# Kernel tuning notes

Measured on AMD Instinct MI355X. Metric: run time of the kernel, lower is better.

The kernel has to match this reference:

```python
import jax, jax.numpy as jnp
import numpy as np

STATE_DIM = 1024
INPUT_DIM = 256
OUTPUT_DIM = 256
KX = 10
LAM = 5.0
BSZ = 16
SEQ = 2048


def setup_inputs() -> dict:
    key = jax.random.key(0)
    ks = jax.random.split(key, 6)
    inputs = jax.random.normal(ks[0], (BSZ, SEQ, INPUT_DIM), dtype=jnp.float32)
    h0 = jax.random.normal(ks[1], (STATE_DIM,), dtype=jnp.float32)
    # exponential_decay_init: entries in (exp(-lam), 1)
    A = jnp.exp(-LAM * jax.random.uniform(ks[2], (STATE_DIM,), dtype=jnp.float32))
    B = jax.random.normal(ks[3], (INPUT_DIM, STATE_DIM), dtype=jnp.float32) / INPUT_DIM
    C = jax.random.normal(ks[4], (STATE_DIM, OUTPUT_DIM), dtype=jnp.float32) / STATE_DIM
    M = jax.random.normal(ks[5], (OUTPUT_DIM, INPUT_DIM, KX), dtype=jnp.float32) / OUTPUT_DIM
    return {"inputs": inputs, "h0": h0, "A": A, "B": B, "C": C, "M": M}


def _lds_forward(inputs, h0, A, B, C, M):
    bsz, L, _ = inputs.shape
    S = A.shape[0]
    kx = M.shape[-1]
    # input projection: u_t @ B  -> [B, L, S]
    uB = jnp.einsum('bld,ds->bls', inputs, B)
    # diagonal linear recurrence h_t = A * h_{t-1} + uB_t, h_{-1} = h0,
    # via parallel associative scan on affine maps (a, b): h -> a*h + b
    a = jnp.broadcast_to(A, (1, L, S))

    def combine(x, y):
        a1, b1 = x
        a2, b2 = y
        return (a1 * a2, a2 * b1 + b2)

    Pa, Pb = jax.lax.associative_scan(combine, (a, uB), axis=1)
    all_h = Pa * h0 + Pb                              # [B, L, S]
    lds_out = jnp.einsum('bls,so->blo', all_h, C)      # [B, L, O]
    # shift forward by kx: new[:, :-kx] = lds_out[:, kx:], tail zeros
    new_lds = jnp.pad(lds_out[:, kx:, :], ((0, 0), (0, kx), (0, 0)))
    # AR term: ar[b,t,o] = sum_{i<kx} M[o,:,i] . x[b, t-i, :] (zero-padded past)
    ar = jnp.zeros_like(new_lds)
    for i in range(kx):
        x_i = jnp.pad(inputs, ((0, 0), (i, 0), (0, 0)))[:, :L, :]
        ar = ar + jnp.einsum('oj,blj->blo', M[:, :, i], x_i)
    return ar + new_lds


def reference(inputs, h0, A, B, C, M):
    return _lds_forward(inputs, h0, A, B, C, M)
```

## Files before the change

kernel.cpp:

```cpp
#include <hip/hip_runtime.h>

#define BSZn 16
#define SEQn 2048
#define DIN 256
#define DST 1024
#define DOUTn 256
#define KXn 10
#define TCH 64
#define NCH 32

typedef __attribute__((ext_vector_type(4))) float f32x4;
typedef __attribute__((ext_vector_type(8))) short bf16x8;

__device__ __forceinline__ unsigned short f2bf(float f){
  unsigned u = __float_as_uint(f);
  u += 0x7FFF + ((u>>16)&1);
  return (unsigned short)(u>>16);
}
__device__ __forceinline__ float bf2f(unsigned short s){
  return __uint_as_float(((unsigned)s)<<16);
}

#define XIDX(r,c) ((((r)<<8) + (c)) ^ (((r)&7)<<3))


__global__ void k_prep(const float* __restrict__ B, const float* __restrict__ C,
                       const float* __restrict__ M, unsigned short* __restrict__ Bt2,
                       unsigned short* __restrict__ Ct2, unsigned short* __restrict__ Mt2){
  int stride = gridDim.x*blockDim.x;
  int i0 = blockIdx.x*blockDim.x + threadIdx.x;
  for(int idx=i0; idx<DIN*DST; idx+=stride){
    int d = idx>>10, s = idx&1023;
    Bt2[((d>>5)<<15) + (s<<5) + (d&31)] = f2bf(B[idx]);
  }
  for(int idx=i0; idx<DST*DOUTn; idx+=stride){
    int s = idx>>8, o = idx&255;
    Ct2[((s>>5)<<13) + (o<<5) + (s&31)] = f2bf(C[idx]);
  }
  for(int idx=i0; idx<DOUTn*DIN*KXn; idx+=stride){
    int q = idx/KXn, ii = idx - q*KXn;
    int o = q>>8, j = q&255;
    int k = (ii<<8) + j;
    Mt2[((k>>5)<<13) + (o<<5) + (k&31)] = f2bf(M[idx]);
  }
}

__global__ __launch_bounds__(256) void k_ub(const float* __restrict__ x,
    const unsigned short* __restrict__ Bt2, const float* __restrict__ A,
    unsigned short* __restrict__ uB, float* __restrict__ P){
  __shared__ __align__(16) unsigned short xt[64*256];
  int wg = blockIdx.x;
  int q = wg & 3, c = (wg>>2)&31, b = wg>>7;
  int t0 = c*TCH, s0 = q<<8;
  const float* xb = x + (size_t)b*SEQn*DIN;
  int tid = threadIdx.x;
  for(int e = tid; e < 64*64; e += 256){
    int r = e>>6, c4 = (e&63)<<2;
    float4 v = *(const float4*)(xb + (t0+r)*DIN + c4);
    ushort4 w; w.x=f2bf(v.x); w.y=f2bf(v.y); w.z=f2bf(v.z); w.w=f2bf(v.w);
    *(ushort4*)&xt[XIDX(r,c4)] = w;
  }
  __syncthreads();
  int wv = tid>>6, ln = tid&63, lm = ln&15, lk = (ln>>4)<<3, rr = (ln>>4)<<2;
  f32x4 zf = {0.f,0.f,0.f,0.f};
  f32x4 acc[4][4];
  #pragma unroll
  for(int tt=0;tt<4;tt++)
    #pragma unroll
    for(int nt=0;nt<4;nt++) acc[tt][nt] = zf;
  #pragma unroll
  for(int kb=0;kb<8;kb++){
    bf16x8 af[4];
    #pragma unroll
    for(int tt=0;tt<4;tt++)
      af[tt] = *(const bf16x8*)&xt[XIDX((tt<<4)+lm, (kb<<5)+lk)];
    #pragma unroll
    for(int nt=0;nt<4;nt++){
      int sg = s0 + (wv<<6) + (nt<<4) + lm;
      bf16x8 bfr = *(const bf16x8*)&Bt2[(kb<<15) + (sg<<5) + lk];
      #pragma unroll
      for(int tt=0;tt<4;tt++)
        acc[tt][nt] = __builtin_amdgcn_mfma_f32_16x16x32_bf16(af[tt], bfr, acc[tt][nt], 0,0,0);
    }
  }
  __syncthreads();
  #pragma unroll
  for(int tt=0;tt<4;tt++)
    #pragma unroll
    for(int nt=0;nt<4;nt++)
      #pragma unroll
      for(int r4=0;r4<4;r4++)
        xt[XIDX((tt<<4)+rr+r4, (wv<<6)+(nt<<4)+lm)] = f2bf(acc[tt][nt][r4]);
  __syncthreads();
  unsigned short* hb = uB + ((size_t)b*129)*32*512;
  #pragma unroll
  for(int it=0; it<8; it++){
    int j = it*256 + tid;
    int r = j>>5, c0 = (j&31)<<3;
    bf16x8 v = *(const bf16x8*)&xt[XIDX(r,c0)];
    int s = s0 + c0;
    size_t addr = (((size_t)(c*4 + (r>>4)))*32 + (s>>5))*512 + ((r&15)<<5) + (s&31);
    *(bf16x8*)&hb[addr] = v;
  }
  if(c == 31){
    unsigned* zp = (unsigned*)(uB + (((size_t)b*129 + 128)*32 + (q<<3))*512);
    for(int e = tid; e < 2048; e += 256) zp[e] = 0u;
  }
  {
    int s = s0 + tid;
    float Av = A[s];
    float p = 0.f;
    #pragma unroll
    for(int t=0;t<64;t++)
      p = fmaf(Av, p, bf2f(xt[XIDX(t, tid)]));
    P[(((b<<5)+c)<<10) + s] = p;
  }
}

__global__ __launch_bounds__(256) void k_h(unsigned short* __restrict__ uB,
    const float* __restrict__ A, const float* __restrict__ h0,
    const float* __restrict__ P){
  int wg = blockIdx.x;
  int half = wg & 1, c = (wg>>1) & 31, b = wg >> 6;
  int tid = threadIdx.x;
  int s = (half<<9) + (tid<<1);
  float2 Av = *(const float2*)(A + s);
  float a0 = Av.x, a1 = Av.y;
  #pragma unroll
  for(int sq=0;sq<6;sq++){ a0 *= a0; a1 *= a1; }
  float2 hv = *(const float2*)(h0 + s);
  float h0v = hv.x, h1v = hv.y;
  const float2* Pb = (const float2*)(P + (((size_t)(b<<5))<<10) + s);
  for(int j=0;j<c;j++){
    float2 pv = Pb[(size_t)j<<9];
    h0v = fmaf(a0, h0v, pv.x);
    h1v = fmaf(a1, h1v, pv.y);
  }
  unsigned short* hb = uB + (((size_t)b*129 + c*4)*32 + (s>>5))*512 + (s&31);
  #pragma unroll 4
  for(int t=0;t<64;t++){
    unsigned* p = (unsigned*)(hb + ((t>>4)*32*512) + ((t&15)<<5));
    unsigned v = *p;
    h0v = fmaf(Av.x, h0v, bf2f((unsigned short)(v & 0xffff)));
    h1v = fmaf(Av.y, h1v, bf2f((unsigned short)(v >> 16)));
    *p = (unsigned)f2bf(h0v) | (((unsigned)f2bf(h1v))<<16);
  }
}

__global__ __launch_bounds__(256,2) void k_arc(const float* __restrict__ x,
    const unsigned short* __restrict__ Mt2, const unsigned short* __restrict__ Ct2,
    const unsigned short* __restrict__ h2, float* __restrict__ out){
  __shared__ __align__(16) unsigned short xt[73*256];
  int wg = blockIdx.x;
  int b = wg>>5, c = wg&31;
  int t0 = c*TCH;
  const float* xb = x + (size_t)b*SEQn*DIN;
  int tid = threadIdx.x;
  for(int e = tid; e < 73*64; e += 256){
    int r = e>>6, c4 = (e&63)<<2;
    int t = t0 - 9 + r;
    float4 v = {0.f,0.f,0.f,0.f};
    if(t >= 0) v = *(const float4*)(xb + t*DIN + c4);
    ushort4 w; w.x=f2bf(v.x); w.y=f2bf(v.y); w.z=f2bf(v.z); w.w=f2bf(v.w);
    *(ushort4*)&xt[XIDX(r, c4)] = w;
  }
  __syncthreads();
  int wv = tid>>6, ln = tid&63, lm = ln&15, lk = (ln>>4)<<3, rr = (ln>>4)<<2;
  f32x4 zf = {0.f,0.f,0.f,0.f};
  f32x4 acc[4][4];
  #pragma unroll
  for(int tt=0;tt<4;tt++)
    #pragma unroll
    for(int nt=0;nt<4;nt++) acc[tt][nt] = zf;
  #pragma unroll 2
  for(int i=0;i<KXn;i++){
    #pragma unroll
    for(int kb8=0;kb8<8;kb8++){
      int col = (kb8<<5) + lk;
      int kq = i*8 + kb8;
      bf16x8 af[4];
      #pragma unroll
      for(int tt=0;tt<4;tt++)
        af[tt] = *(const bf16x8*)&xt[XIDX((tt<<4)+lm + 9 - i, col)];
      #pragma unroll
      for(int nt=0;nt<4;nt++){
        int o = (wv<<6) + (nt<<4) + lm;
        bf16x8 bfr = *(const bf16x8*)&Mt2[(kq<<13) + (o<<5) + lk];
        #pragma unroll
        for(int tt=0;tt<4;tt++)
          acc[tt][nt] = __builtin_amdgcn_mfma_f32_16x16x32_bf16(af[tt], bfr, acc[tt][nt], 0,0,0);
      }
    }
  }
  const unsigned short* hb = h2 + (size_t)b*129*32*512;
  int Tg0 = c*4 + (lm>=6 ? 1 : 0);
  int rowin = (lm<6) ? (10+lm) : (lm-6);
  #pragma unroll
  for(int kb=0;kb<32;kb++){
    bf16x8 af[4];
    #pragma unroll
    for(int tt=0;tt<4;tt++)
      af[tt] = *(const bf16x8*)&hb[(((size_t)(Tg0+tt))*32 + kb)*512 + rowin*32 + lk];
    #pragma unroll
    for(int nt=0;nt<4;nt++){
      int o = (wv<<6) + (nt<<4) + lm;
      bf16x8 bfr = *(const bf16x8*)&Ct2[(kb<<13) + (o<<5) + lk];
      #pragma unroll
      for(int tt=0;tt<4;tt++)
        acc[tt][nt] = __builtin_amdgcn_mfma_f32_16x16x32_bf16(af[tt], bfr, acc[tt][nt], 0,0,0);
    }
  }
  #pragma unroll
  for(int tt=0;tt<4;tt++)
    #pragma unroll
    for(int nt=0;nt<4;nt++)
      #pragma unroll
      for(int r4=0;r4<4;r4++){
        int m = (tt<<4) + rr + r4;
        int o = (wv<<6) + (nt<<4) + lm;
        out[((size_t)b*SEQn + t0 + m)*DOUTn + o] = acc[tt][nt][r4];
      }
}

extern "C" void kernel_launch(void* const* d_in, const int* in_sizes, int n_in,
                              void* d_out, int out_size, void* d_ws, size_t ws_size,
                              hipStream_t stream){
  const float* x  = (const float*)d_in[0];
  const float* h0 = (const float*)d_in[1];
  const float* A  = (const float*)d_in[2];
  const float* B  = (const float*)d_in[3];
  const float* C  = (const float*)d_in[4];
  const float* M  = (const float*)d_in[5];
  float* out = (float*)d_out;
  unsigned short* Bt2 = (unsigned short*)d_ws;
  unsigned short* Ct2 = Bt2 + DIN*DST;
  unsigned short* Mt2 = Ct2 + DST*DOUTn;
  float* P     = (float*)((char*)d_ws + ( 4u<<20));
  unsigned short* uB = (unsigned short*)((char*)d_ws + (8u<<20));
  k_prep <<<512, 256, 0, stream>>>(B, C, M, Bt2, Ct2, Mt2);
  k_ub   <<<BSZn*NCH*4, 256, 0, stream>>>(x, Bt2, A, uB, P);
  k_h    <<<BSZn*NCH*2, 256, 0, stream>>>(uB, A, h0, P);
  k_arc  <<<BSZn*NCH, 256, 0, stream>>>(x, Mt2, Ct2, uB, out);
}
```

Baseline: 255.8 us.

## Reuse x tile across state quarters in k_ub and double-buffer global loads in k_arc

k_ub now has each workgroup loop over all four 256-wide state quarters, so the x tile is loaded and converted to bf16 once instead of four times. Results are staged in a separate LDS buffer, which doubles shared memory per block and cuts the grid by 4x, lowering parallelism. In k_arc, the M and C/h operand loads from global memory are software-pipelined with explicit ping-pong register buffers so they overlap the MFMA work. This raises register pressure under the launch_bounds(256,2) limit.

```diff
diff --git a/kernel.cpp b/kernel.cpp
--- a/kernel.cpp
+++ b/kernel.cpp
@@ -49,9 +49,10 @@
     const unsigned short* __restrict__ Bt2, const float* __restrict__ A,
     unsigned short* __restrict__ uB, float* __restrict__ P){
   __shared__ __align__(16) unsigned short xt[64*256];
+  __shared__ __align__(16) unsigned short ub[64*256];
   int wg = blockIdx.x;
-  int q = wg & 3, c = (wg>>2)&31, b = wg>>7;
-  int t0 = c*TCH, s0 = q<<8;
+  int c = wg & 31, b = wg >> 5;
+  int t0 = c*TCH;
   const float* xb = x + (size_t)b*SEQn*DIN;
   int tid = threadIdx.x;
   for(int e = tid; e < 64*64; e += 256){
@@ -62,58 +63,61 @@
   }
   __syncthreads();
   int wv = tid>>6, ln = tid&63, lm = ln&15, lk = (ln>>4)<<3, rr = (ln>>4)<<2;
+  unsigned short* hb = uB + ((size_t)b*129)*32*512;
   f32x4 zf = {0.f,0.f,0.f,0.f};
-  f32x4 acc[4][4];
-  #pragma unroll
-  for(int tt=0;tt<4;tt++)
-    #pragma unroll
-    for(int nt=0;nt<4;nt++) acc[tt][nt] = zf;
-  #pragma unroll
-  for(int kb=0;kb<8;kb++){
-    bf16x8 af[4];
+  for(int q=0;q<4;q++){
+    int s0 = q<<8;
+    f32x4 acc[4][4];
     #pragma unroll
     for(int tt=0;tt<4;tt++)
-      af[tt] = *(const bf16x8*)&xt[XIDX((tt<<4)+lm, (kb<<5)+lk)];
-    #pragma unroll
-    for(int nt=0;nt<4;nt++){
-      int sg = s0 + (wv<<6) + (nt<<4) + lm;
-      bf16x8 bfr = *(const bf16x8*)&Bt2[(kb<<15) + (sg<<5) + lk];
+      #pragma unroll
+      for(int nt=0;nt<4;nt++) acc[tt][nt] = zf;
+    #pragma unroll
+    for(int kb=0;kb<8;kb++){
+      bf16x8 af[4];
       #pragma unroll
       for(int tt=0;tt<4;tt++)
-        acc[tt][nt] = __builtin_amdgcn_mfma_f32_16x16x32_bf16(af[tt], bfr, acc[tt][nt], 0,0,0);
+        af[tt] = *(const bf16x8*)&xt[XIDX((tt<<4)+lm, (kb<<5)+lk)];
+      #pragma unroll
+      for(int nt=0;nt<4;nt++){
+        int sg = s0 + (wv<<6) + (nt<<4) + lm;
+        bf16x8 bfr = *(const bf16x8*)&Bt2[(kb<<15) + (sg<<5) + lk];
+        #pragma unroll
+        for(int tt=0;tt<4;tt++)
+          acc[tt][nt] = __builtin_amdgcn_mfma_f32_16x16x32_bf16(af[tt], bfr, acc[tt][nt], 0,0,0);
+      }
     }
-  }
-  __syncthreads();
-  #pragma unroll
-  for(int tt=0;tt<4;tt++)
-    #pragma unroll
-    for(int nt=0;nt<4;nt++)
-      #pragma unroll
-      for(int r4=0;r4<4;r4++)
-        xt[XIDX((tt<<4)+rr+r4, (wv<<6)+(nt<<4)+lm)] = f2bf(acc[tt][nt][r4]);
-  __syncthreads();
-  unsigned short* hb = uB + ((size_t)b*129)*32*512;
-  #pragma unroll
-  for(int it=0; it<8; it++){
-    int j = it*256 + tid;
-    int r = j>>5, c0 = (j&31)<<3;
-    bf16x8 v = *(const bf16x8*)&xt[XIDX(r,c0)];
-    int s = s0 + c0;
-    size_t addr = (((size_t)(c*4 + (r>>4)))*32 + (s>>5))*512 + ((r&15)<<5) + (s&31);
-    *(bf16x8*)&hb[addr] = v;
+    __syncthreads();
+    #pragma unroll
+    for(int tt=0;tt<4;tt++)
+      #pragma unroll
+      for(int nt=0;nt<4;nt++)
+        #pragma unroll
+        for(int r4=0;r4<4;r4++)
+          ub[XIDX((tt<<4)+rr+r4, (wv<<6)+(nt<<4)+lm)] = f2bf(acc[tt][nt][r4]);
+    __syncthreads();
+    #pragma unroll
+    for(int it=0; it<8; it++){
+      int j = it*256 + tid;
+      int r = j>>5, c0 = (j&31)<<3;
+      bf16x8 v = *(const bf16x8*)&ub[XIDX(r,c0)];
+      int s = s0 + c0;
+      size_t addr = (((size_t)(c*4 + (r>>4)))*32 + (s>>5))*512 + ((r&15)<<5) + (s&31);
+      *(bf16x8*)&hb[addr] = v;
+    }
+    {
+      int s = s0 + tid;
+      float Av = A[s];
+      float p = 0.f;
+      #pragma unroll
+      for(int t=0;t<64;t++)
+        p = fmaf(Av, p, bf2f(ub[XIDX(t, tid)]));
+      P[(((b<<5)+c)<<10) + s] = p;
+    }
   }
   if(c == 31){
-    unsigned* zp = (unsigned*)(uB + (((size_t)b*129 + 128)*32 + (q<<3))*512);
-    for(int e = tid; e < 2048; e += 256) zp[e] = 0u;
-  }
-  {
-    int s = s0 + tid;
-    float Av = A[s];
-    float p = 0.f;
-    #pragma unroll
-    for(int t=0;t<64;t++)
-      p = fmaf(Av, p, bf2f(xt[XIDX(t, tid)]));
-    P[(((b<<5)+c)<<10) + s] = p;
+    unsigned* zp = (unsigned*)(uB + (((size_t)b*129 + 128)*32)*512);
+    for(int e = tid; e < 8192; e += 256) zp[e] = 0u;
   }
 }
 
@@ -172,44 +176,53 @@
   for(int tt=0;tt<4;tt++)
     #pragma unroll
     for(int nt=0;nt<4;nt++) acc[tt][nt] = zf;
-  #pragma unroll 2
-  for(int i=0;i<KXn;i++){
-    #pragma unroll
-    for(int kb8=0;kb8<8;kb8++){
-      int col = (kb8<<5) + lk;
-      int kq = i*8 + kb8;
-      bf16x8 af[4];
-      #pragma unroll
-      for(int tt=0;tt<4;tt++)
-        af[tt] = *(const bf16x8*)&xt[XIDX((tt<<4)+lm + 9 - i, col)];
-      #pragma unroll
-      for(int nt=0;nt<4;nt++){
-        int o = (wv<<6) + (nt<<4) + lm;
-        bf16x8 bfr = *(const bf16x8*)&Mt2[(kq<<13) + (o<<5) + lk];
-        #pragma unroll
-        for(int tt=0;tt<4;tt++)
-          acc[tt][nt] = __builtin_amdgcn_mfma_f32_16x16x32_bf16(af[tt], bfr, acc[tt][nt], 0,0,0);
-      }
-    }
-  }
+
+  const unsigned short* mb = Mt2 + ((((wv<<6)+lm)<<5) + lk);
+  bf16x8 pA[8], pB[8];
+#define LOADG(buf, IT0) { _Pragma("unroll") \
+    for(int j=0;j<8;j++){ int itt=(IT0)+(j>>2); \
+      buf[j] = *(const bf16x8*)&mb[((size_t)itt<<13) + ((j&3)<<9)]; } }
+#define COMPG(buf, IT0) { _Pragma("unroll") \
+    for(int jj=0;jj<2;jj++){ int itc=(IT0)+jj; int ii=itc>>3, k8=itc&7; \
+      int col=(k8<<5)+lk; bf16x8 af[4]; \
+      _Pragma("unroll") for(int tt=0;tt<4;tt++) \
+        af[tt] = *(const bf16x8*)&xt[XIDX((tt<<4)+lm+9-ii, col)]; \
+      _Pragma("unroll") for(int nt=0;nt<4;nt++){ \
+        _Pragma("unroll") for(int tt=0;tt<4;tt++) \
+          acc[tt][nt] = __builtin_amdgcn_mfma_f32_16x16x32_bf16(af[tt], buf[jj*4+nt], acc[tt][nt],0,0,0); } } }
+  LOADG(pA, 0)
+  for(int g=0; g<80; g+=4){
+    LOADG(pB, g+2)
+    COMPG(pA, g)
+    if(g+4 < 80) LOADG(pA, g+4)
+    COMPG(pB, g+2)
+  }
+
   const unsigned short* hb = h2 + (size_t)b*129*32*512;
   int Tg0 = c*4 + (lm>=6 ? 1 : 0);
   int rowin = (lm<6) ? (10+lm) : (lm-6);
-  #pragma unroll
-  for(int kb=0;kb<32;kb++){
-    bf16x8 af[4];
-    #pragma unroll
-    for(int tt=0;tt<4;tt++)
-      af[tt] = *(const bf16x8*)&hb[(((size_t)(Tg0+tt))*32 + kb)*512 + rowin*32 + lk];
-    #pragma unroll
-    for(int nt=0;nt<4;nt++){
-      int o = (wv<<6) + (nt<<4) + lm;
-      bf16x8 bfr = *(const bf16x8*)&Ct2[(kb<<13) + (o<<5) + lk];
-      #pragma unroll
-      for(int tt=0;tt<4;tt++)
-        acc[tt][nt] = __builtin_amdgcn_mfma_f32_16x16x32_bf16(af[tt], bfr, acc[tt][nt], 0,0,0);
-    }
-  }
+  const unsigned short* hp[4];
+  #pragma unroll
+  for(int tt=0;tt<4;tt++)
+    hp[tt] = hb + (((size_t)(Tg0+tt)*32)<<9) + rowin*32 + lk;
+  const unsigned short* cb = Ct2 + ((((wv<<6)+lm)<<5) + lk);
+  bf16x8 qa[4], qb4[4], qaf[4], qbf[4];
+#define CLOADG(bufA, bufB, KB) { _Pragma("unroll") \
+    for(int tt=0;tt<4;tt++) bufA[tt] = *(const bf16x8*)&hp[tt][((size_t)(KB))<<9]; \
+    _Pragma("unroll") \
+    for(int nt=0;nt<4;nt++) bufB[nt] = *(const bf16x8*)&cb[(((size_t)(KB))<<13) + (nt<<9)]; }
+#define CCOMP(bufA, bufB) { _Pragma("unroll") \
+    for(int nt=0;nt<4;nt++) \
+      _Pragma("unroll") for(int tt=0;tt<4;tt++) \
+        acc[tt][nt] = __builtin_amdgcn_mfma_f32_16x16x32_bf16(bufA[tt], bufB[nt], acc[tt][nt],0,0,0); }
+  CLOADG(qaf, qbf, 0)
+  for(int kb=0; kb<32; kb+=2){
+    CLOADG(qa, qb4, kb+1)
+    CCOMP(qaf, qbf)
+    if(kb+2 < 32) CLOADG(qaf, qbf, kb+2)
+    CCOMP(qa, qb4)
+  }
+
   #pragma unroll
   for(int tt=0;tt<4;tt++)
     #pragma unroll
@@ -238,7 +251,7 @@
   float* P     = (float*)((char*)d_ws + ( 4u<<20));
   unsigned short* uB = (unsigned short*)((char*)d_ws + (8u<<20));
   k_prep <<<512, 256, 0, stream>>>(B, C, M, Bt2, Ct2, Mt2);
-  k_ub   <<<BSZn*NCH*4, 256, 0, stream>>>(x, Bt2, A, uB, P);
+  k_ub   <<<BSZn*NCH, 256, 0, stream>>>(x, Bt2, A, uB, P);
   k_h    <<<BSZn*NCH*2, 256, 0, stream>>>(uB, A, h0, P);
   k_arc  <<<BSZn*NCH, 256, 0, stream>>>(x, Mt2, Ct2, uB, out);
 }
```

New measurement: 252.2 us. Within noise of the previous version (-1.4%).

## Stage weight tiles into LDS via async global_load_lds with double buffering

Applied to the files above, without the earlier changes.

Reorganizes the B, M and C weights into swizzled 8K-element tiles, with M and C concatenated into one stream. k_ub and k_arc now copy each tile into LDS with global_load_lds while the previous tile feeds MFMA, instead of reading weight fragments directly from global memory. k_ub is also restructured so one block handles all four state quarters and reuses its converted x tile, cutting the grid by four. This trades direct global loads for a barrier on every k-step, extra LDS use, and lower parallelism in k_ub.

```diff
diff --git a/kernel.cpp b/kernel.cpp
--- a/kernel.cpp
+++ b/kernel.cpp
@@ -20,38 +20,49 @@
 __device__ __forceinline__ float bf2f(unsigned short s){
   return __uint_as_float(((unsigned)s)<<16);
 }
+__device__ __forceinline__ void gl_lds16(const unsigned short* g, unsigned short* l){
+  __builtin_amdgcn_global_load_lds(
+      (const __attribute__((address_space(1))) void*)g,
+      (__attribute__((address_space(3))) void*)l, 16, 0, 0);
+}
 
 #define XIDX(r,c) ((((r)<<8) + (c)) ^ (((r)&7)<<3))
 
 
+
 __global__ void k_prep(const float* __restrict__ B, const float* __restrict__ C,
-                       const float* __restrict__ M, unsigned short* __restrict__ Bt2,
-                       unsigned short* __restrict__ Ct2, unsigned short* __restrict__ Mt2){
+                       const float* __restrict__ M, unsigned short* __restrict__ Ut,
+                       unsigned short* __restrict__ Wt){
   int stride = gridDim.x*blockDim.x;
   int i0 = blockIdx.x*blockDim.x + threadIdx.x;
   for(int idx=i0; idx<DIN*DST; idx+=stride){
     int d = idx>>10, s = idx&1023;
-    Bt2[((d>>5)<<15) + (s<<5) + (d&31)] = f2bf(B[idx]);
-  }
-  for(int idx=i0; idx<DST*DOUTn; idx+=stride){
-    int s = idx>>8, o = idx&255;
-    Ct2[((s>>5)<<13) + (o<<5) + (s&31)] = f2bf(C[idx]);
+    int sl = s&255, kl = d&31;
+    Ut[(size_t)(((s>>8)<<3)+(d>>5))*8192 + (sl<<5) + ((((kl>>3))^(sl&3))<<3) + (kl&7)]
+      = f2bf(B[idx]);
   }
   for(int idx=i0; idx<DOUTn*DIN*KXn; idx+=stride){
     int q = idx/KXn, ii = idx - q*KXn;
     int o = q>>8, j = q&255;
-    int k = (ii<<8) + j;
-    Mt2[((k>>5)<<13) + (o<<5) + (k&31)] = f2bf(M[idx]);
+    int kq = ii*8 + (j>>5), kl = j&31;
+    Wt[(size_t)kq*8192 + (o<<5) + (((kl>>3)^(o&3))<<3) + (kl&7)] = f2bf(M[idx]);
+  }
+  for(int idx=i0; idx<DST*DOUTn; idx+=stride){
+    int s = idx>>8, o = idx&255;
+    int kq = 80 + (s>>5), kl = s&31;
+    Wt[(size_t)kq*8192 + (o<<5) + (((kl>>3)^(o&3))<<3) + (kl&7)] = f2bf(C[idx]);
   }
 }
 
 __global__ __launch_bounds__(256) void k_ub(const float* __restrict__ x,
-    const unsigned short* __restrict__ Bt2, const float* __restrict__ A,
+    const unsigned short* __restrict__ Ut, const float* __restrict__ A,
     unsigned short* __restrict__ uB, float* __restrict__ P){
   __shared__ __align__(16) unsigned short xt[64*256];
+  __shared__ __align__(16) unsigned short sh[2][8192];
+  unsigned short* ubp = &sh[0][0];
   int wg = blockIdx.x;
-  int q = wg & 3, c = (wg>>2)&31, b = wg>>7;
-  int t0 = c*TCH, s0 = q<<8;
+  int c = wg & 31, b = wg >> 5;
+  int t0 = c*TCH;
   const float* xb = x + (size_t)b*SEQn*DIN;
   int tid = threadIdx.x;
   for(int e = tid; e < 64*64; e += 256){
@@ -60,60 +71,76 @@
     ushort4 w; w.x=f2bf(v.x); w.y=f2bf(v.y); w.z=f2bf(v.z); w.w=f2bf(v.w);
     *(ushort4*)&xt[XIDX(r,c4)] = w;
   }
-  __syncthreads();
   int wv = tid>>6, ln = tid&63, lm = ln&15, lk = (ln>>4)<<3, rr = (ln>>4)<<2;
+  int swz = ((ln>>4) ^ (lm&3)) << 3;
+  unsigned short* hb = uB + ((size_t)b*129)*32*512;
   f32x4 zf = {0.f,0.f,0.f,0.f};
-  f32x4 acc[4][4];
-  #pragma unroll
-  for(int tt=0;tt<4;tt++)
-    #pragma unroll
-    for(int nt=0;nt<4;nt++) acc[tt][nt] = zf;
-  #pragma unroll
-  for(int kb=0;kb<8;kb++){
-    bf16x8 af[4];
+  for(int q=0;q<4;q++){
+    int s0 = q<<8;
+    __syncthreads();
+    {
+      const unsigned short* src = Ut + (size_t)(q<<3)*8192;
+      #pragma unroll
+      for(int i=0;i<4;i++){ int ci=(i<<2)+wv; gl_lds16(src+ci*512+ln*8, &sh[0][ci*512]); }
+    }
+    __syncthreads();
+    f32x4 acc[4][4];
     #pragma unroll
     for(int tt=0;tt<4;tt++)
-      af[tt] = *(const bf16x8*)&xt[XIDX((tt<<4)+lm, (kb<<5)+lk)];
-    #pragma unroll
-    for(int nt=0;nt<4;nt++){
-      int sg = s0 + (wv<<6) + (nt<<4) + lm;
-      bf16x8 bfr = *(const bf16x8*)&Bt2[(kb<<15) + (sg<<5) + lk];
+      #pragma unroll
+      for(int nt=0;nt<4;nt++) acc[tt][nt] = zf;
+    int cur = 0;
+    for(int kb=0;kb<8;kb++){
+      if(kb<7){
+        const unsigned short* src = Ut + (size_t)((q<<3)+kb+1)*8192;
+        #pragma unroll
+        for(int i=0;i<4;i++){ int ci=(i<<2)+wv; gl_lds16(src+ci*512+ln*8, &sh[cur^1][ci*512]); }
+      }
+      bf16x8 af[4], bfr[4];
       #pragma unroll
       for(int tt=0;tt<4;tt++)
-        acc[tt][nt] = __builtin_amdgcn_mfma_f32_16x16x32_bf16(af[tt], bfr, acc[tt][nt], 0,0,0);
-    }
-  }
-  __syncthreads();
-  #pragma unroll
-  for(int tt=0;tt<4;tt++)
-    #pragma unroll
-    for(int nt=0;nt<4;nt++)
-      #pragma unroll
-      for(int r4=0;r4<4;r4++)
-        xt[XIDX((tt<<4)+rr+r4, (wv<<6)+(nt<<4)+lm)] = f2bf(acc[tt][nt][r4]);
-  __syncthreads();
-  unsigned short* hb = uB + ((size_t)b*129)*32*512;
-  #pragma unroll
-  for(int it=0; it<8; it++){
-    int j = it*256 + tid;
-    int r = j>>5, c0 = (j&31)<<3;
-    bf16x8 v = *(const bf16x8*)&xt[XIDX(r,c0)];
-    int s = s0 + c0;
-    size_t addr = (((size_t)(c*4 + (r>>4)))*32 + (s>>5))*512 + ((r&15)<<5) + (s&31);
-    *(bf16x8*)&hb[addr] = v;
+        af[tt] = *(const bf16x8*)&xt[XIDX((tt<<4)+lm, (kb<<5)+lk)];
+      #pragma unroll
+      for(int nt=0;nt<4;nt++)
+        bfr[nt] = *(const bf16x8*)&sh[cur][(((wv<<6)+(nt<<4)+lm)<<5) + swz];
+      #pragma unroll
+      for(int nt=0;nt<4;nt++)
+        #pragma unroll
+        for(int tt=0;tt<4;tt++)
+          acc[tt][nt] = __builtin_amdgcn_mfma_f32_16x16x32_bf16(af[tt], bfr[nt], acc[tt][nt], 0,0,0);
+      __syncthreads();
+      cur ^= 1;
+    }
+    #pragma unroll
+    for(int tt=0;tt<4;tt++)
+      #pragma unroll
+      for(int nt=0;nt<4;nt++)
+        #pragma unroll
+        for(int r4=0;r4<4;r4++)
+          ubp[XIDX((tt<<4)+rr+r4, (wv<<6)+(nt<<4)+lm)] = f2bf(acc[tt][nt][r4]);
+    __syncthreads();
+    #pragma unroll
+    for(int it=0; it<8; it++){
+      int j = it*256 + tid;
+      int r = j>>5, c0 = (j&31)<<3;
+      bf16x8 v = *(const bf16x8*)&ubp[XIDX(r,c0)];
+      int s = s0 + c0;
+      size_t addr = (((size_t)(c*4 + (r>>4)))*32 + (s>>5))*512 + ((r&15)<<5) + (s&31);
+      *(bf16x8*)&hb[addr] = v;
+    }
+    {
+      int s = s0 + tid;
+      float Av = A[s];
+      float p = 0.f;
+      #pragma unroll
+      for(int t=0;t<64;t++)
+        p = fmaf(Av, p, bf2f(ubp[XIDX(t, tid)]));
+      P[(((b<<5)+c)<<10) + s] = p;
+    }
   }
   if(c == 31){
-    unsigned* zp = (unsigned*)(uB + (((size_t)b*129 + 128)*32 + (q<<3))*512);
-    for(int e = tid; e < 2048; e += 256) zp[e] = 0u;
-  }
-  {
-    int s = s0 + tid;
-    float Av = A[s];
-    float p = 0.f;
-    #pragma unroll
-    for(int t=0;t<64;t++)
-      p = fmaf(Av, p, bf2f(xt[XIDX(t, tid)]));
-    P[(((b<<5)+c)<<10) + s] = p;
+    unsigned* zp = (unsigned*)(uB + (((size_t)b*129 + 128)*32)*512);
+    for(int e = tid; e < 8192; e += 256) zp[e] = 0u;
   }
 }
 
@@ -147,15 +174,18 @@
   }
 }
 
-__global__ __launch_bounds__(256,2) void k_arc(const float* __restrict__ x,
-    const unsigned short* __restrict__ Mt2, const unsigned short* __restrict__ Ct2,
-    const unsigned short* __restrict__ h2, float* __restrict__ out){
+__global__ __launch_bounds__(256) void k_arc(const float* __restrict__ x,
+    const unsigned short* __restrict__ Wt, const unsigned short* __restrict__ h2,
+    float* __restrict__ out){
   __shared__ __align__(16) unsigned short xt[73*256];
+  __shared__ __align__(16) unsigned short wb[2][8192];
   int wg = blockIdx.x;
   int b = wg>>5, c = wg&31;
   int t0 = c*TCH;
   const float* xb = x + (size_t)b*SEQn*DIN;
   int tid = threadIdx.x;
+  int wv = tid>>6, ln = tid&63, lm = ln&15, lk = (ln>>4)<<3, rr = (ln>>4)<<2;
+  int swz = ((ln>>4) ^ (lm&3)) << 3;
   for(int e = tid; e < 73*64; e += 256){
     int r = e>>6, c4 = (e&63)<<2;
     int t = t0 - 9 + r;
@@ -164,51 +194,91 @@
     ushort4 w; w.x=f2bf(v.x); w.y=f2bf(v.y); w.z=f2bf(v.z); w.w=f2bf(v.w);
     *(ushort4*)&xt[XIDX(r, c4)] = w;
   }
+  {
+    #pragma unroll
+    for(int i=0;i<4;i++){ int ci=(i<<2)+wv; gl_lds16(Wt+ci*512+ln*8, &wb[0][ci*512]); }
+  }
   __syncthreads();
-  int wv = tid>>6, ln = tid&63, lm = ln&15, lk = (ln>>4)<<3, rr = (ln>>4)<<2;
   f32x4 zf = {0.f,0.f,0.f,0.f};
   f32x4 acc[4][4];
   #pragma unroll
   for(int tt=0;tt<4;tt++)
     #pragma unroll
     for(int nt=0;nt<4;nt++) acc[tt][nt] = zf;
-  #pragma unroll 2
-  for(int i=0;i<KXn;i++){
-    #pragma unroll
-    for(int kb8=0;kb8<8;kb8++){
-      int col = (kb8<<5) + lk;
-      int kq = i*8 + kb8;
-      bf16x8 af[4];
+  int cur = 0;
+  for(int kq=0;kq<80;kq++){
+    {
+      const unsigned short* src = Wt + (size_t)(kq+1)*8192;
+      #pragma unroll
+      for(int i=0;i<4;i++){ int ci=(i<<2)+wv; gl_lds16(src+ci*512+ln*8, &wb[cur^1][ci*512]); }
+    }
+    int ii = kq>>3, k8 = kq&7, col = (k8<<5)+lk;
+    bf16x8 af[4], bfr[4];
+    #pragma unroll
+    for(int tt=0;tt<4;tt++)
+      af[tt] = *(const bf16x8*)&xt[XIDX((tt<<4)+lm+9-ii, col)];
+    #pragma unroll
+    for(int nt=0;nt<4;nt++)
+      bfr[nt] = *(const bf16x8*)&wb[cur][(((wv<<6)+(nt<<4)+lm)<<5) + swz];
+    #pragma unroll
+    for(int nt=0;nt<4;nt++)
       #pragma unroll
       for(int tt=0;tt<4;tt++)
-        af[tt] = *(const bf16x8*)&xt[XIDX((tt<<4)+lm + 9 - i, col)];
-      #pragma unroll
-      for(int nt=0;nt<4;nt++){
-        int o = (wv<<6) + (nt<<4) + lm;
-        bf16x8 bfr = *(const bf16x8*)&Mt2[(kq<<13) + (o<<5) + lk];
-        #pragma unroll
-        for(int tt=0;tt<4;tt++)
-          acc[tt][nt] = __builtin_amdgcn_mfma_f32_16x16x32_bf16(af[tt], bfr, acc[tt][nt], 0,0,0);
-      }
-    }
+        acc[tt][nt] = __builtin_amdgcn_mfma_f32_16x16x32_bf16(af[tt], bfr[nt], acc[tt][nt], 0,0,0);
+    __syncthreads();
+    cur ^= 1;
   }
   const unsigned short* hb = h2 + (size_t)b*129*32*512;
   int Tg0 = c*4 + (lm>=6 ? 1 : 0);
   int rowin = (lm<6) ? (10+lm) : (lm-6);
-  #pragma unroll
-  for(int kb=0;kb<32;kb++){
-    bf16x8 af[4];
-    #pragma unroll
-    for(int tt=0;tt<4;tt++)
-      af[tt] = *(const bf16x8*)&hb[(((size_t)(Tg0+tt))*32 + kb)*512 + rowin*32 + lk];
-    #pragma unroll
-    for(int nt=0;nt<4;nt++){
-      int o = (wv<<6) + (nt<<4) + lm;
-      bf16x8 bfr = *(const bf16x8*)&Ct2[(kb<<13) + (o<<5) + lk];
-      #pragma unroll
-      for(int tt=0;tt<4;tt++)
-        acc[tt][nt] = __builtin_amdgcn_mfma_f32_16x16x32_bf16(af[tt], bfr, acc[tt][nt], 0,0,0);
-    }
+  const unsigned short* hp[4];
+  #pragma unroll
+  for(int tt=0;tt<4;tt++)
+    hp[tt] = hb + (((size_t)(Tg0+tt)*32)<<9) + rowin*32 + lk;
+  bf16x8 hEv[4], hOd[4];
+  #pragma unroll
+  for(int tt=0;tt<4;tt++) hEv[tt] = *(const bf16x8*)&hp[tt][0];
+  for(int kb2=0; kb2<32; kb2+=2){
+    {
+      const unsigned short* src = Wt + (size_t)(81+kb2)*8192;
+      #pragma unroll
+      for(int i=0;i<4;i++){ int ci=(i<<2)+wv; gl_lds16(src+ci*512+ln*8, &wb[cur^1][ci*512]); }
+    }
+    #pragma unroll
+    for(int tt=0;tt<4;tt++) hOd[tt] = *(const bf16x8*)&hp[tt][(size_t)(kb2+1)<<9];
+    {
+      bf16x8 bfr[4];
+      #pragma unroll
+      for(int nt=0;nt<4;nt++)
+        bfr[nt] = *(const bf16x8*)&wb[cur][(((wv<<6)+(nt<<4)+lm)<<5) + swz];
+      #pragma unroll
+      for(int nt=0;nt<4;nt++)
+        #pragma unroll
+        for(int tt=0;tt<4;tt++)
+          acc[tt][nt] = __builtin_amdgcn_mfma_f32_16x16x32_bf16(hEv[tt], bfr[nt], acc[tt][nt], 0,0,0);
+    }
+    __syncthreads();
+    cur ^= 1;
+    if(kb2+2 < 32){
+      const unsigned short* src = Wt + (size_t)(82+kb2)*8192;
+      #pragma unroll
+      for(int i=0;i<4;i++){ int ci=(i<<2)+wv; gl_lds16(src+ci*512+ln*8, &wb[cur^1][ci*512]); }
+      #pragma unroll
+      for(int tt=0;tt<4;tt++) hEv[tt] = *(const bf16x8*)&hp[tt][(size_t)(kb2+2)<<9];
+    }
+    {
+      bf16x8 bfr[4];
+      #pragma unroll
+      for(int nt=0;nt<4;nt++)
+        bfr[nt] = *(const bf16x8*)&wb[cur][(((wv<<6)+(nt<<4)+lm)<<5) + swz];
+      #pragma unroll
+      for(int nt=0;nt<4;nt++)
+        #pragma unroll
+        for(int tt=0;tt<4;tt++)
+          acc[tt][nt] = __builtin_amdgcn_mfma_f32_16x16x32_bf16(hOd[tt], bfr[nt], acc[tt][nt], 0,0,0);
+    }
+    __syncthreads();
+    cur ^= 1;
   }
   #pragma unroll
   for(int tt=0;tt<4;tt++)
@@ -232,13 +302,12 @@
   const float* C  = (const float*)d_in[4];
   const float* M  = (const float*)d_in[5];
   float* out = (float*)d_out;
-  unsigned short* Bt2 = (unsigned short*)d_ws;
-  unsigned short* Ct2 = Bt2 + DIN*DST;
-  unsigned short* Mt2 = Ct2 + DST*DOUTn;
-  float* P     = (float*)((char*)d_ws + ( 4u<<20));
+  unsigned short* Ut = (unsigned short*)d_ws;
+  unsigned short* Wt = (unsigned short*)((char*)d_ws + (1u<<20));
+  float* P     = (float*)((char*)d_ws + (4u<<20));
   unsigned short* uB = (unsigned short*)((char*)d_ws + (8u<<20));
-  k_prep <<<512, 256, 0, stream>>>(B, C, M, Bt2, Ct2, Mt2);
-  k_ub   <<<BSZn*NCH*4, 256, 0, stream>>>(x, Bt2, A, uB, P);
+  k_prep <<<512, 256, 0, stream>>>(B, C, M, Ut, Wt);
+  k_ub   <<<BSZn*NCH, 256, 0, stream>>>(x, Ut, A, uB, P);
   k_h    <<<BSZn*NCH*2, 256, 0, stream>>>(uB, A, h0, P);
-  k_arc  <<<BSZn*NCH, 256, 0, stream>>>(x, Mt2, Ct2, uB, out);
-}
+  k_arc  <<<BSZn*NCH, 256, 0, stream>>>(x, Wt, uB, out);
+}
```

Measured after the change: 250.4 us. 2.1% less time.
